# Kernel tuning notes

Hardware: AMD Instinct MI355X
Metric: run time of the kernel (lower is better)

## Reference

```python
import jax, jax.numpy as jnp
import numpy as np

D_MODEL = 1024
NUM_HEADS = 16
D_HEAD = 64  # d_q = d_k = d_v
BATCH = 4
SEQ = 2048


def _trunc_normal(key, shape, std):
    # truncated normal in [-3*std, 3*std], matching nn.init.trunc_normal_
    return jax.random.truncated_normal(key, -3.0, 3.0, shape, dtype=jnp.float32) * std


def setup_inputs() -> dict:
    key = jax.random.key(0)
    k_x, k_q, k_k, k_v, k_o = jax.random.split(key, 5)
    hd = NUM_HEADS * D_HEAD
    s_in = np.sqrt(2.0 / (D_MODEL + hd))
    s_out = np.sqrt(2.0 / (hd + D_MODEL))
    return {
        "in_features": jax.random.normal(k_x, (BATCH, SEQ, D_MODEL), dtype=jnp.float32),
        "w_q": _trunc_normal(k_q, (hd, D_MODEL), s_in),
        "w_k": _trunc_normal(k_k, (hd, D_MODEL), s_in),
        "w_v": _trunc_normal(k_v, (hd, D_MODEL), s_in),
        "w_o": _trunc_normal(k_o, (D_MODEL, hd), s_out),
    }


def reference(in_features, w_q, w_k, w_v, w_o):
    B, S, D = in_features.shape
    H, Dh = NUM_HEADS, D_HEAD
    # QKV projections (weight stored as [out, in])
    q = jnp.einsum('od,bsd->bso', w_q, in_features).reshape(B, S, H, Dh).transpose(0, 2, 1, 3)
    k = jnp.einsum('od,bsd->bso', w_k, in_features).reshape(B, S, H, Dh).transpose(0, 2, 1, 3)
    v = jnp.einsum('od,bsd->bso', w_v, in_features).reshape(B, S, H, Dh).transpose(0, 2, 1, 3)
    # scaled dot-product attention with dense causal mask (as in source)
    att = jnp.einsum('bhqd,bhkd->bhqk', q, k) / jnp.sqrt(jnp.float32(Dh)).astype(q.dtype)
    causal = jnp.tril(jnp.ones((S, S), dtype=bool))
    att = jnp.where(causal, att, -jnp.inf)
    att = jax.nn.softmax(att, axis=-1)
    out = jnp.einsum('bhqk,bhkd->bhqd', att, v)  # [B,H,S,Dh]
    out = out.transpose(0, 2, 1, 3).reshape(B, S, H * Dh)
    return jnp.einsum('od,bsd->bso', w_o, out)
```

## Files before the change

kernel.cpp:

```cpp
#include <hip/hip_runtime.h>
#include <stdint.h>

#define D_MODEL 1024
#define NHEADS  16
#define DHEAD   64
#define BATCH   4
#define SEQ     2048
#define MTOT    (BATCH*SEQ)

typedef unsigned short u16;
typedef uint32_t u32;
typedef __bf16 bf16x8 __attribute__((ext_vector_type(8)));
typedef float  f32x4  __attribute__((ext_vector_type(4)));
typedef float  f32x16 __attribute__((ext_vector_type(16)));
typedef u16    u16x8  __attribute__((ext_vector_type(8)));
typedef u16    u16x4  __attribute__((ext_vector_type(4)));
typedef u32    u32x4  __attribute__((ext_vector_type(4)));

__device__ __forceinline__ u16 f2bf(float f) {
  uint32_t u = __builtin_bit_cast(uint32_t, f);
  u += 0x7fff + ((u >> 16) & 1);
  return (u16)(u >> 16);
}

__device__ __forceinline__ void gll16(const u16* g, u16* lds) {
  __builtin_amdgcn_global_load_lds(
      (__attribute__((address_space(1))) void*)(g),
      (__attribute__((address_space(3))) void*)(lds), 16, 0, 0);
}

__global__ void cvtk(const float4* __restrict__ in, u16x4* __restrict__ out, int n4) {
  const int i = blockIdx.x * blockDim.x + threadIdx.x;
  if (i < n4) {
    const float4 f = in[i];
    u16x4 h;
    h[0] = f2bf(f.x); h[1] = f2bf(f.y); h[2] = f2bf(f.z); h[3] = f2bf(f.w);
    out[i] = h;
  }
}

__global__ void cvtk4(const float4* __restrict__ a, const float4* __restrict__ b,
                      const float4* __restrict__ c, const float4* __restrict__ d,
                      u16x4* __restrict__ out, int n4) {
  const int i = blockIdx.x * blockDim.x + threadIdx.x;
  if (i >= n4) return;
  const float4* src = (blockIdx.y == 0) ? a : (blockIdx.y == 1) ? b
                    : (blockIdx.y == 2) ? c : d;
  const float4 f = src[i];
  u16x4 h;
  h[0] = f2bf(f.x); h[1] = f2bf(f.y); h[2] = f2bf(f.z); h[3] = f2bf(f.w);
  out[(size_t)blockIdx.y * n4 + i] = h;
}

#define QS 8192

#define BARS() __builtin_amdgcn_s_barrier()
#define LGKM0() do { asm volatile("s_waitcnt lgkmcnt(0)" ::: "memory"); \
                     __builtin_amdgcn_sched_barrier(0); } while (0)

#define STG(pbase, roff, t_, slot_) do {                                        \
    gll16((pbase) + (size_t)(roff)*1024 + (t_)*64,      qsm + (slot_)*QS + w*512);        \
    gll16((pbase) + (size_t)((roff)+64)*1024 + (t_)*64, qsm + (slot_)*QS + w*512 + 4096); \
  } while (0)

#define PH_READS_A() do {                                                       \
    _Pragma("unroll")                                                           \
    for (int mf = 0; mf < 8; ++mf) {                                            \
      af0[mf] = *(const bf16x8*)&sA[(mf*16 + r15)*64 + cs0];                    \
      af1[mf] = *(const bf16x8*)&sA[(mf*16 + r15)*64 + cs1];                    \
    }                                                                           \
    _Pragma("unroll")                                                           \
    for (int nf = 0; nf < 4; ++nf)                                              \
      bq[nf] = *(const bf16x8*)&sB[(brow + nf*16 + r15)*64 + cs0];              \
  } while (0)

#define PH_READS_B1() do {                                                      \
    _Pragma("unroll")                                                           \
    for (int nf = 0; nf < 4; ++nf)                                              \
      bq[nf] = *(const bf16x8*)&sB[(brow + nf*16 + r15)*64 + cs1];              \
  } while (0)

#define MM(AF, N0, N1) do {                                                     \
    __builtin_amdgcn_s_setprio(1);                                              \
    _Pragma("unroll")                                                           \
    for (int mf = 0; mf < 8; ++mf) {                                            \
      acc[mf][N0] = __builtin_amdgcn_mfma_f32_16x16x32_bf16(AF[mf], bq[N0],     \
                                                            acc[mf][N0], 0,0,0);\
      acc[mf][N1] = __builtin_amdgcn_mfma_f32_16x16x32_bf16(AF[mf], bq[N1],     \
                                                            acc[mf][N1], 0,0,0);\
    }                                                                           \
    __builtin_amdgcn_s_setprio(0);                                              \
  } while (0)

__global__ __launch_bounds__(512, 2) void gemm_qkv8p(
    const u16* __restrict__ A, const u16* __restrict__ Bw, u16* __restrict__ Out)
{
  extern __shared__ u16 qsm[];
  const int tid = threadIdx.x;
  const int w = tid >> 6, l = tid & 63;
  const int wm = w >> 2, wn = w & 3;
  const int bid = blockIdx.x;
  const int wg = (bid & 7) * 48 + (bid >> 3);
  const int m0 = (wg / 12) * 256, n0 = (wg % 12) * 256;

  const int sr  = 8*w + (l >> 3);
  const int sc8 = ((l & 7) ^ ((l >> 3) & 7)) * 8;
  const u16* pA = A  + (size_t)(m0 + sr) * 1024 + sc8;
  const u16* pB = Bw + (size_t)(n0 + sr) * 1024 + sc8;

  const int r15 = l & 15;
  const int cs0 = (((l >> 4) + 0) ^ (l & 7)) * 8;
  const int cs1 = (((l >> 4) + 4) ^ (l & 7)) * 8;
  const int brow = (wn & 1) * 64;

  f32x4 acc[8][4];
  #pragma unroll
  for (int i = 0; i < 8; ++i)
    #pragma unroll
    for (int j = 0; j < 4; ++j)
      acc[i][j] = f32x4{0.f, 0.f, 0.f, 0.f};

  STG(pA, 0,   0, 0);
  STG(pA, 128, 0, 1);
  STG(pB, 0,   0, 2);
  STG(pB, 128, 0, 3);
  STG(pA, 0,   1, 4);
  STG(pA, 128, 1, 5);
  STG(pB, 0,   1, 6);
  asm volatile("s_waitcnt vmcnt(6)" ::: "memory");
  BARS();
  __builtin_amdgcn_sched_barrier(0);

  #pragma unroll 2
  for (int t = 0; t < 14; ++t) {
    const int p = t & 1, po = p ^ 1;
    const u16* sA = qsm + (size_t)(p*4 + wm) * QS;
    const u16* sB = qsm + (size_t)(p*4 + 2 + (wn >> 1)) * QS;
    bf16x8 af0[8], af1[8], bq[4];
    PH_READS_A();
    STG(pB, 128, t+1, po*4 + 3);
    BARS(); LGKM0();
    MM(af0, 0, 1);
    BARS();
    STG(pA, 0, t+2, p*4 + 0);
    BARS();
    MM(af0, 2, 3);
    BARS();
    PH_READS_B1();
    STG(pA, 128, t+2, p*4 + 1);
    BARS(); LGKM0();
    MM(af1, 0, 1);
    BARS();
    STG(pB, 0, t+2, p*4 + 2);
    BARS();
    MM(af1, 2, 3);
    asm volatile("s_waitcnt vmcnt(6)" ::: "memory");
    BARS();
    __builtin_amdgcn_sched_barrier(0);
  }

  {
    const u16* sA = qsm + (size_t)(0*4 + wm) * QS;
    const u16* sB = qsm + (size_t)(0*4 + 2 + (wn >> 1)) * QS;
    bf16x8 af0[8], af1[8], bq[4];
    PH_READS_A();
    STG(pB, 128, 15, 4 + 3);
    BARS(); LGKM0();
    MM(af0, 0, 1);
    BARS();
    BARS();
    MM(af0, 2, 3);
    BARS();
    PH_READS_B1();
    BARS(); LGKM0();
    MM(af1, 0, 1);
    BARS();
    MM(af1, 2, 3);
    asm volatile("s_waitcnt vmcnt(0)" ::: "memory");
    BARS();
    __builtin_amdgcn_sched_barrier(0);
  }
  {
    const u16* sA = qsm + (size_t)(1*4 + wm) * QS;
    const u16* sB = qsm + (size_t)(1*4 + 2 + (wn >> 1)) * QS;
    bf16x8 af0[8], af1[8], bq[4];
    PH_READS_A();
    MM(af0, 0, 1);
    MM(af0, 2, 3);
    PH_READS_B1();
    MM(af1, 0, 1);
    MM(af1, 2, 3);
  }

  const float scale = (n0 < 1024) ? 0.125f * 1.44269504088896f : 1.0f;
  const int g = l >> 4, c15 = l & 15;
  #pragma unroll
  for (int mf = 0; mf < 8; ++mf) {
    #pragma unroll
    for (int nf = 0; nf < 4; ++nf) {
      #pragma unroll
      for (int j = 0; j < 4; ++j) {
        const int row = m0 + wm*128 + mf*16 + g*4 + j;
        const int col = n0 + wn*64 + nf*16 + c15;
        const int z = col >> 10;
        const int wi = col & 1023;
        const int b = row >> 11, sq = row & (SEQ-1);
        const int h = wi >> 6, dh = wi & (DHEAD-1);
        Out[(size_t)z * MTOT * D_MODEL
            + ((size_t)(b*NHEADS + h) * SEQ + sq) * DHEAD + dh] =
            f2bf(acc[mf][nf][j] * scale);
      }
    }
  }
}

#undef STG
#undef PH_READS_A
#undef PH_READS_B1
#undef MM

#define OSTG(pbase, roff, t_, slot_) do {                                       \
    gll16((pbase) + (size_t)(roff)*1024 + (t_)*64,      osm + (slot_)*QS + w*512);        \
    gll16((pbase) + (size_t)((roff)+64)*1024 + (t_)*64, osm + (slot_)*QS + w*512 + 4096); \
  } while (0)

#define OREADS_P1() do {                                                        \
    _Pragma("unroll")                                                           \
    for (int mf = 0; mf < 8; ++mf) {                                            \
      af0[mf] = *(const bf16x8*)&sA[(mf*16 + r15)*64 + cs0];                    \
      af1[mf] = *(const bf16x8*)&sA[(mf*16 + r15)*64 + cs1];                    \
    }                                                                           \
    _Pragma("unroll")                                                           \
    for (int nf = 0; nf < 2; ++nf)                                              \
      bq[nf] = *(const bf16x8*)&sB[(brow + nf*16 + r15)*64 + cs0];              \
  } while (0)

#define OREADS_P2() do {                                                        \
    _Pragma("unroll")                                                           \
    for (int nf = 0; nf < 2; ++nf)                                              \
      bq[nf] = *(const bf16x8*)&sB[(brow + nf*16 + r15)*64 + cs1];              \
  } while (0)

#define OMM(AF) do {                                                            \
    __builtin_amdgcn_s_setprio(1);                                              \
    _Pragma("unroll")                                                           \
    for (int mf = 0; mf < 8; ++mf) {                                            \
      acc[mf][0] = __builtin_amdgcn_mfma_f32_16x16x32_bf16(AF[mf], bq[0],       \
                                                           acc[mf][0], 0,0,0);  \
      acc[mf][1] = __builtin_amdgcn_mfma_f32_16x16x32_bf16(AF[mf], bq[1],       \
                                                           acc[mf][1], 0,0,0);  \
    }                                                                           \
    __builtin_amdgcn_s_setprio(0);                                              \
  } while (0)

__global__ __launch_bounds__(512, 2) void gemm_o8p(
    const u16* __restrict__ A, const u16* __restrict__ Bw, float* __restrict__ Out)
{
  extern __shared__ u16 osm[];
  const int tid = threadIdx.x;
  const int w = tid >> 6, l = tid & 63;
  const int wm = w >> 2, wn = w & 3;
  const int bid = blockIdx.x;
  const int wg = (bid & 7) * 32 + (bid >> 3);
  const int m0 = (wg >> 3) * 256, n0 = (wg & 7) * 128;

  const int sr  = 8*w + (l >> 3);
  const int sc8 = ((l & 7) ^ ((l >> 3) & 7)) * 8;
  const u16* pA = A  + (size_t)(m0 + sr) * 1024 + sc8;
  const u16* pB = Bw + (size_t)(n0 + sr) * 1024 + sc8;

  const int r15 = l & 15;
  const int cs0 = (((l >> 4) + 0) ^ (l & 7)) * 8;
  const int cs1 = (((l >> 4) + 4) ^ (l & 7)) * 8;
  const int brow = wn * 32;

  f32x4 acc[8][2];
  #pragma unroll
  for (int i = 0; i < 8; ++i) {
    acc[i][0] = f32x4{0.f, 0.f, 0.f, 0.f};
    acc[i][1] = f32x4{0.f, 0.f, 0.f, 0.f};
  }

  OSTG(pA, 0,   0, 0);
  OSTG(pA, 128, 0, 1);
  OSTG(pB, 0,   0, 2);
  OSTG(pA, 0,   1, 3);
  OSTG(pA, 128, 1, 4);
  asm volatile("s_waitcnt vmcnt(4)" ::: "memory");
  BARS();
  __builtin_amdgcn_sched_barrier(0);

  #pragma unroll 2
  for (int t = 0; t < 14; ++t) {
    const int p = t & 1, po = p ^ 1;
    const u16* sA = osm + (size_t)(p*3 + wm) * QS;
    const u16* sB = osm + (size_t)(p*3 + 2) * QS;
    bf16x8 af0[8], af1[8], bq[2];
    OREADS_P1();
    OSTG(pB, 0, t+1, po*3 + 2);
    BARS(); LGKM0();
    OMM(af0);
    BARS();
    OREADS_P2();
    OSTG(pA, 0,   t+2, p*3 + 0);
    OSTG(pA, 128, t+2, p*3 + 1);
    BARS(); LGKM0();
    OMM(af1);
    asm volatile("s_waitcnt vmcnt(4)" ::: "memory");
    BARS();
    __builtin_amdgcn_sched_barrier(0);
  }

  {
    const u16* sA = osm + (size_t)(0*3 + wm) * QS;
    const u16* sB = osm + (size_t)(0*3 + 2) * QS;
    bf16x8 af0[8], af1[8], bq[2];
    OREADS_P1();
    OSTG(pB, 0, 15, 1*3 + 2);
    BARS(); LGKM0();
    OMM(af0);
    BARS();
    OREADS_P2();
    BARS(); LGKM0();
    OMM(af1);
    asm volatile("s_waitcnt vmcnt(0)" ::: "memory");
    BARS();
    __builtin_amdgcn_sched_barrier(0);
  }
  {
    const u16* sA = osm + (size_t)(1*3 + wm) * QS;
    const u16* sB = osm + (size_t)(1*3 + 2) * QS;
    bf16x8 af0[8], af1[8], bq[2];
    OREADS_P1();
    OMM(af0);
    OREADS_P2();
    OMM(af1);
  }

  const int g = l >> 4, c15 = l & 15;
  #pragma unroll
  for (int mf = 0; mf < 8; ++mf) {
    #pragma unroll
    for (int nf = 0; nf < 2; ++nf) {
      #pragma unroll
      for (int j = 0; j < 4; ++j) {
        const int row = m0 + wm*128 + mf*16 + g*4 + j;
        const int col = n0 + wn*32 + nf*16 + c15;
        Out[(size_t)row * D_MODEL + col] = acc[mf][nf][j];
      }
    }
  }
}

#undef OSTG
#undef OREADS_P1
#undef OREADS_P2
#undef OMM

__launch_bounds__(512, 2)
__global__ void attn6_k(const u16* __restrict__ Qb, const u16* __restrict__ Kb_,
                        const u16* __restrict__ Vb_, u16* __restrict__ Oa)
{
  const int tid = threadIdx.x;
  const int w = tid >> 6, l = tid & 63;
  const int q5 = l & 31, hi = l >> 5;
  const int r = blockIdx.x;
  const int bh = (r & 7) * 8 + ((r >> 3) & 7);
  const int pairi = r >> 6;
  const int b = bh >> 4, h = bh & 15;
  const size_t base = (size_t)bh * SEQ * DHEAD;
  const u16* Qg = Qb + base;
  const u16* Kg = Kb_ + base;
  const u16* Vg = Vb_ + base;

  __shared__ __align__(16) u16 smem[32768];

  const int kc = tid & 7, rp = tid >> 3;
  const int vsub = rp >> 5;
  const int rp5 = rp & 31;
  int vIdx32[8];
  #pragma unroll
  for (int e = 0; e < 8; ++e)
    vIdx32[e] = vsub*2048 + (8*kc + e)*32 + ((((rp5 >> 2) ^ kc ^ e) & 7) << 2) + (rp5 & 3);

  const int kr8 = l >> 3;
  const int kkv = 8*w + kr8;
  const int kdc = (l & 7) ^ kr8 ^ w;

  for (int half = 0; half < 2; ++half) {
    const int tq = half ? (7 - pairi) : pairi;
    const int q0w = tq*256 + 32*w;
    const int ntk = (tq + 1) * 2;
    const int ntw = (q0w >> 7) + 1;

    bf16x8 qf[4];
    #pragma unroll
    for (int s = 0; s < 4; ++s)
      qf[s] = *(const bf16x8*)(Qg + (size_t)(q0w + q5)*DHEAD + 16*s + 8*hi);

    f32x16 c0 = {}, c1 = {};
    float mrun = -1e30f, lrun = 0.f;

    {
      #pragma unroll
      for (int h2 = 0; h2 < 2; ++h2)
        gll16(Kg + (size_t)(64*h2 + kkv)*DHEAD + kdc*8, smem + h2*4096 + w*512);
      const u16x8 v0 = *(const u16x8*)(Vg + (size_t)(2*rp)*DHEAD + kc*8);
      const u16x8 v1 = *(const u16x8*)(Vg + (size_t)(2*rp + 1)*DHEAD + kc*8);
      u32* Vd = (u32*)(smem + 16384);
      #pragma unroll
      for (int e = 0; e < 8; ++e)
        Vd[vIdx32[e]] = (u32)v0[e] | ((u32)v1[e] << 16);
    }
    __syncthreads();

    for (int t = 0; t < ntk; ++t) {
      const int cur = t & 1;
      const bool pf = (t + 1 < ntk);
      u16x8 v0, v1;
      if (pf) {
        const int kv1 = (t + 1) * 128;
        v0 = *(const u16x8*)(Vg + (size_t)(kv1 + 2*rp)*DHEAD + kc*8);
        v1 = *(const u16x8*)(Vg + (size_t)(kv1 + 2*rp + 1)*DHEAD + kc*8);
        #pragma unroll
        for (int h2 = 0; h2 < 2; ++h2)
          gll16(Kg + (size_t)(kv1 + 64*h2 + kkv)*DHEAD + kdc*8,
                smem + (cur^1)*8192 + h2*4096 + w*512);
      }

      if (t < ntw) {
        const u16* Kb = smem + cur*8192;
        const u16* Vv = smem + 16384 + cur*8192;

        f32x16 st[4] = {{}, {}, {}, {}};
        __builtin_amdgcn_s_setprio(1);
        #pragma unroll
        for (int kbg = 0; kbg < 4; ++kbg) {
          #pragma unroll
          for (int s = 0; s < 4; ++s) {
            const int slot = ((2*s + hi) ^ (l & 7) ^ ((4*(kbg & 1)) & 7) ^ (q5 >> 3)) & 7;
            const bf16x8 kf = *(const bf16x8*)(Kb + (kbg >> 1)*4096
                                               + ((kbg & 1)*32 + q5)*64 + slot*8);
            st[kbg] = __builtin_amdgcn_mfma_f32_32x32x16_bf16(kf, qf[s], st[kbg], 0, 0, 0);
          }
        }
        __builtin_amdgcn_s_setprio(0);

        if (t == ntw - 1) {
          const int kv0 = t * 128;
          #pragma unroll
          for (int kbg = 0; kbg < 4; ++kbg)
            #pragma unroll
            for (int rr = 0; rr < 16; ++rr) {
              const int kvg = kv0 + 32*kbg + (rr & 3) + 8*(rr >> 2) + 4*hi;
              if (kvg > q0w + q5) st[kbg][rr] = -1e30f;
            }
        }

        float mx = -1e30f;
        #pragma unroll
        for (int kbg = 0; kbg < 4; ++kbg)
          #pragma unroll
          for (int rr = 0; rr < 16; ++rr) mx = fmaxf(mx, st[kbg][rr]);
        mx = fmaxf(mx, __shfl_xor(mx, 32));
        float alpha = 1.0f;
        if (!__all(mx <= mrun + 8.0f)) {
          const float mnew = fmaxf(mrun, mx);
          alpha = __builtin_amdgcn_exp2f(mrun - mnew);
          mrun = mnew;
          #pragma unroll
          for (int rr = 0; rr < 16; ++rr) { c0[rr] *= alpha; c1[rr] *= alpha; }
        }
        float rs = 0.f;
        #pragma unroll
        for (int kbg = 0; kbg < 4; ++kbg)
          #pragma unroll
          for (int rr = 0; rr < 16; ++rr) {
            const float pe = __builtin_amdgcn_exp2f(st[kbg][rr] - mrun);
            st[kbg][rr] = pe;
            rs += pe;
          }
        rs += __shfl_xor(rs, 32);
        lrun = lrun * alpha + rs;

        bf16x8 pb[8];
        #pragma unroll
        for (int kbg = 0; kbg < 4; ++kbg) {
          u32 pw[8];
          #pragma unroll
          for (int i = 0; i < 8; ++i) {
            u32 t0;
            asm("v_cvt_pk_bf16_f32 %0, %1, %2"
                : "=v"(t0) : "v"(st[kbg][2*i]), "v"(st[kbg][2*i+1]));
            pw[i] = t0;
          }
          asm("v_permlane32_swap_b32 %0, %1" : "+v"(pw[0]), "+v"(pw[2]));
          asm("v_permlane32_swap_b32 %0, %1" : "+v"(pw[1]), "+v"(pw[3]));
          asm("v_permlane32_swap_b32 %0, %1" : "+v"(pw[4]), "+v"(pw[6]));
          asm("v_permlane32_swap_b32 %0, %1" : "+v"(pw[5]), "+v"(pw[7]));
          pb[2*kbg]   = __builtin_bit_cast(bf16x8, u32x4{pw[0], pw[1], pw[2], pw[3]});
          pb[2*kbg+1] = __builtin_bit_cast(bf16x8, u32x4{pw[4], pw[5], pw[6], pw[7]});
        }

        __builtin_amdgcn_s_setprio(1);
        #pragma unroll
        for (int h2 = 0; h2 < 2; ++h2) {
          #pragma unroll
          for (int s = 0; s < 4; ++s) {
            {
              const int slot = ((2*s + hi) ^ (l & 7) ^ (q5 >> 3)) & 7;
              const bf16x8 vf = *(const bf16x8*)(Vv + h2*4096 + q5*64 + slot*8);
              c0 = __builtin_amdgcn_mfma_f32_32x32x16_bf16(vf, pb[4*h2 + s], c0, 0, 0, 0);
            }
            {
              const int slot = ((2*s + hi) ^ (l & 7) ^ 4 ^ (q5 >> 3)) & 7;
              const bf16x8 vf = *(const bf16x8*)(Vv + h2*4096 + (32 + q5)*64 + slot*8);
              c1 = __builtin_amdgcn_mfma_f32_32x32x16_bf16(vf, pb[4*h2 + s], c1, 0, 0, 0);
            }
          }
        }
        __builtin_amdgcn_s_setprio(0);
      }

      if (pf) {
        u32* Vd = (u32*)(smem + 16384) + (cur^1)*4096;
        #pragma unroll
        for (int e = 0; e < 8; ++e)
          Vd[vIdx32[e]] = (u32)v0[e] | ((u32)v1[e] << 16);
      }
      __syncthreads();
    }

    const float linv = __builtin_amdgcn_rcpf(lrun);
    #pragma unroll
    for (int Ab = 0; Ab < 2; ++Ab)
      #pragma unroll
      for (int rr = 0; rr < 16; ++rr) {
        const int d = 32*Ab + (rr & 3) + 8*(rr >> 2) + 4*hi;
        smem[w*2048 + q5*64 + (((d >> 3) ^ (q5 & 7)) & 7)*8 + (d & 7)] =
            f2bf((Ab ? c1[rr] : c0[rr]) * linv);
      }
    __syncthreads();
    #pragma unroll
    for (int cc = 0; cc < 4; ++cc) {
      const int dchunk = 4*hi + cc;
      const u16x8 vv = *(const u16x8*)&smem[w*2048 + q5*64 + ((dchunk ^ (q5 & 7)) & 7)*8];
      *(u16x8*)(Oa + (size_t)(b*SEQ + q0w + q5)*D_MODEL + h*DHEAD + 32*hi + 8*cc) = vv;
    }
    __syncthreads();
  }
}

extern "C" void kernel_launch(void* const* d_in, const int* in_sizes, int n_in,
                              void* d_out, int out_size, void* d_ws, size_t ws_size,
                              hipStream_t stream) {
  const float* X  = (const float*)d_in[0];
  const float* Wq = (const float*)d_in[1];
  const float* Wk = (const float*)d_in[2];
  const float* Wv = (const float*)d_in[3];
  const float* Wo = (const float*)d_in[4];

  u16* xb  = (u16*)d_ws;
  u16* wqb = xb  + (size_t)MTOT*D_MODEL;
  u16* wkb = wqb + (size_t)D_MODEL*D_MODEL;
  u16* wvb = wkb + (size_t)D_MODEL*D_MODEL;
  u16* wob = wvb + (size_t)D_MODEL*D_MODEL;
  u16* qkv = wob + (size_t)D_MODEL*D_MODEL;
  u16* att = qkv + (size_t)3*MTOT*D_MODEL;

  (void)hipFuncSetAttribute((const void*)gemm_qkv8p,
                            hipFuncAttributeMaxDynamicSharedMemorySize, 131072);
  (void)hipFuncSetAttribute((const void*)gemm_o8p,
                            hipFuncAttributeMaxDynamicSharedMemorySize, 98304);

  const int nx4 = MTOT*D_MODEL/4;
  const int nw4 = D_MODEL*D_MODEL/4;
  cvtk<<<nx4/256, 256, 0, stream>>>((const float4*)X, (u16x4*)xb, nx4);
  dim3 gc(nw4/256, 4, 1);
  cvtk4<<<gc, 256, 0, stream>>>((const float4*)Wq, (const float4*)Wk,
                                (const float4*)Wv, (const float4*)Wo,
                                (u16x4*)wqb, nw4);

  gemm_qkv8p<<<384, 512, 131072, stream>>>(xb, wqb, qkv);

  attn6_k<<<256, 512, 0, stream>>>(qkv, qkv + (size_t)MTOT*D_MODEL,
                                   qkv + (size_t)2*MTOT*D_MODEL, att);

  gemm_o8p<<<256, 512, 98304, stream>>>(att, wob, (float*)d_out);
}
```

Measured before the change: 153.7 us.

## Retile QKV projection GEMM to 256x192 tiles with 512 workgroups

Changes the fused QKV GEMM tile from 256x256 to 256x192, so the grid grows from 384 to 512 workgroups and fills the 256 CUs in two full waves of 2 blocks per CU, instead of leaving a partial wave. The staging pipeline is restructured: B tiles are loaded as 192 rows per stage with 3 loads per wave, the inner k-step merges into two MFMA phases with fewer barriers, and LDS per block drops to 112KB. The per-column Q scale is now chosen per output column, because a 192-wide tile can straddle the Q/K boundary. Per-tile arithmetic intensity is slightly lower and global traffic for the A operand is higher in exchange for better wave balance.

```diff
diff --git a/kernel.cpp b/kernel.cpp
--- a/kernel.cpp
+++ b/kernel.cpp
@@ -53,46 +53,52 @@
 }
 
 #define QS 8192
-
 #define BARS() __builtin_amdgcn_s_barrier()
 #define LGKM0() do { asm volatile("s_waitcnt lgkmcnt(0)" ::: "memory"); \
                      __builtin_amdgcn_sched_barrier(0); } while (0)
 
-#define STG(pbase, roff, t_, slot_) do {                                        \
-    gll16((pbase) + (size_t)(roff)*1024 + (t_)*64,      qsm + (slot_)*QS + w*512);        \
-    gll16((pbase) + (size_t)((roff)+64)*1024 + (t_)*64, qsm + (slot_)*QS + w*512 + 4096); \
-  } while (0)
-
-#define PH_READS_A() do {                                                       \
-    _Pragma("unroll")                                                           \
-    for (int mf = 0; mf < 8; ++mf) {                                            \
-      af0[mf] = *(const bf16x8*)&sA[(mf*16 + r15)*64 + cs0];                    \
-      af1[mf] = *(const bf16x8*)&sA[(mf*16 + r15)*64 + cs1];                    \
-    }                                                                           \
-    _Pragma("unroll")                                                           \
-    for (int nf = 0; nf < 4; ++nf)                                              \
-      bq[nf] = *(const bf16x8*)&sB[(brow + nf*16 + r15)*64 + cs0];              \
-  } while (0)
-
-#define PH_READS_B1() do {                                                      \
-    _Pragma("unroll")                                                           \
-    for (int nf = 0; nf < 4; ++nf)                                              \
-      bq[nf] = *(const bf16x8*)&sB[(brow + nf*16 + r15)*64 + cs1];              \
-  } while (0)
-
-#define MM(AF, N0, N1) do {                                                     \
-    __builtin_amdgcn_s_setprio(1);                                              \
-    _Pragma("unroll")                                                           \
-    for (int mf = 0; mf < 8; ++mf) {                                            \
-      acc[mf][N0] = __builtin_amdgcn_mfma_f32_16x16x32_bf16(AF[mf], bq[N0],     \
-                                                            acc[mf][N0], 0,0,0);\
-      acc[mf][N1] = __builtin_amdgcn_mfma_f32_16x16x32_bf16(AF[mf], bq[N1],     \
-                                                            acc[mf][N1], 0,0,0);\
-    }                                                                           \
-    __builtin_amdgcn_s_setprio(0);                                              \
-  } while (0)
-
-__global__ __launch_bounds__(512, 2) void gemm_qkv8p(
+#define QP3 28672
+
+#define Q3_ASTG(roff, t_, dstoff) do {                                            \
+    gll16(pA + (size_t)(roff)*1024 + (t_)*64,      qsm + (dstoff) + w*512);       \
+    gll16(pA + (size_t)((roff)+64)*1024 + (t_)*64, qsm + (dstoff) + w*512 + 4096);\
+  } while (0)
+
+#define Q3_BSTG(t_, dstoff) do {                                                  \
+    gll16(pB + (size_t)0*1024  + (t_)*64, qsm + (dstoff) + w*1536);               \
+    gll16(pB + (size_t)8*1024  + (t_)*64, qsm + (dstoff) + w*1536 + 512);         \
+    gll16(pB + (size_t)16*1024 + (t_)*64, qsm + (dstoff) + w*1536 + 1024);        \
+  } while (0)
+
+#define Q3_READS_P1() do {                                                        \
+    _Pragma("unroll")                                                             \
+    for (int mf = 0; mf < 8; ++mf) {                                              \
+      af0[mf] = *(const bf16x8*)&sA[(mf*16 + r15)*64 + cs0];                      \
+      af1[mf] = *(const bf16x8*)&sA[(mf*16 + r15)*64 + cs1];                      \
+    }                                                                             \
+    _Pragma("unroll")                                                             \
+    for (int nf = 0; nf < 3; ++nf)                                                \
+      bq[nf] = *(const bf16x8*)&sB[(brow + nf*16 + r15)*64 + cs0];                \
+  } while (0)
+
+#define Q3_READS_P2() do {                                                        \
+    _Pragma("unroll")                                                             \
+    for (int nf = 0; nf < 3; ++nf)                                                \
+      bq[nf] = *(const bf16x8*)&sB[(brow + nf*16 + r15)*64 + cs1];                \
+  } while (0)
+
+#define Q3_MM(AF) do {                                                            \
+    __builtin_amdgcn_s_setprio(1);                                                \
+    _Pragma("unroll")                                                             \
+    for (int mf = 0; mf < 8; ++mf)                                                \
+      _Pragma("unroll")                                                           \
+      for (int nf = 0; nf < 3; ++nf)                                              \
+        acc[mf][nf] = __builtin_amdgcn_mfma_f32_16x16x32_bf16(AF[mf], bq[nf],     \
+                                                              acc[mf][nf], 0,0,0);\
+    __builtin_amdgcn_s_setprio(0);                                                \
+  } while (0)
+
+__global__ __launch_bounds__(512, 2) void gemm_qkv192(
     const u16* __restrict__ A, const u16* __restrict__ Bw, u16* __restrict__ Out)
 {
   extern __shared__ u16 qsm[];
@@ -100,110 +106,94 @@
   const int w = tid >> 6, l = tid & 63;
   const int wm = w >> 2, wn = w & 3;
   const int bid = blockIdx.x;
-  const int wg = (bid & 7) * 48 + (bid >> 3);
-  const int m0 = (wg / 12) * 256, n0 = (wg % 12) * 256;
-
-  const int sr  = 8*w + (l >> 3);
+  const int wg = (bid & 7) * 64 + (bid >> 3);
+  const int m0 = (wg >> 4) * 256, n0 = (wg & 15) * 192;
+
   const int sc8 = ((l & 7) ^ ((l >> 3) & 7)) * 8;
-  const u16* pA = A  + (size_t)(m0 + sr) * 1024 + sc8;
-  const u16* pB = Bw + (size_t)(n0 + sr) * 1024 + sc8;
+  const u16* pA = A  + (size_t)(m0 + 8*w  + (l >> 3)) * 1024 + sc8;
+  const u16* pB = Bw + (size_t)(n0 + 24*w + (l >> 3)) * 1024 + sc8;
 
   const int r15 = l & 15;
   const int cs0 = (((l >> 4) + 0) ^ (l & 7)) * 8;
   const int cs1 = (((l >> 4) + 4) ^ (l & 7)) * 8;
-  const int brow = (wn & 1) * 64;
-
-  f32x4 acc[8][4];
+  const int brow = wn * 48;
+
+  f32x4 acc[8][3];
   #pragma unroll
   for (int i = 0; i < 8; ++i)
     #pragma unroll
-    for (int j = 0; j < 4; ++j)
+    for (int j = 0; j < 3; ++j)
       acc[i][j] = f32x4{0.f, 0.f, 0.f, 0.f};
 
-  STG(pA, 0,   0, 0);
-  STG(pA, 128, 0, 1);
-  STG(pB, 0,   0, 2);
-  STG(pB, 128, 0, 3);
-  STG(pA, 0,   1, 4);
-  STG(pA, 128, 1, 5);
-  STG(pB, 0,   1, 6);
-  asm volatile("s_waitcnt vmcnt(6)" ::: "memory");
+  Q3_ASTG(0,   0, 0);
+  Q3_ASTG(128, 0, 8192);
+  Q3_BSTG(0, 16384);
+  Q3_ASTG(0,   1, QP3 + 0);
+  Q3_ASTG(128, 1, QP3 + 8192);
+  asm volatile("s_waitcnt vmcnt(4)" ::: "memory");
   BARS();
   __builtin_amdgcn_sched_barrier(0);
 
   #pragma unroll 2
   for (int t = 0; t < 14; ++t) {
     const int p = t & 1, po = p ^ 1;
-    const u16* sA = qsm + (size_t)(p*4 + wm) * QS;
-    const u16* sB = qsm + (size_t)(p*4 + 2 + (wn >> 1)) * QS;
-    bf16x8 af0[8], af1[8], bq[4];
-    PH_READS_A();
-    STG(pB, 128, t+1, po*4 + 3);
-    BARS(); LGKM0();
-    MM(af0, 0, 1);
-    BARS();
-    STG(pA, 0, t+2, p*4 + 0);
-    BARS();
-    MM(af0, 2, 3);
-    BARS();
-    PH_READS_B1();
-    STG(pA, 128, t+2, p*4 + 1);
-    BARS(); LGKM0();
-    MM(af1, 0, 1);
-    BARS();
-    STG(pB, 0, t+2, p*4 + 2);
-    BARS();
-    MM(af1, 2, 3);
-    asm volatile("s_waitcnt vmcnt(6)" ::: "memory");
+    const u16* sA = qsm + (size_t)p*QP3 + (size_t)wm*8192;
+    const u16* sB = qsm + (size_t)p*QP3 + 16384;
+    bf16x8 af0[8], af1[8], bq[3];
+    Q3_READS_P1();
+    Q3_BSTG(t+1, po*QP3 + 16384);
+    BARS(); LGKM0();
+    Q3_MM(af0);
+    BARS();
+    Q3_READS_P2();
+    Q3_ASTG(0,   t+2, p*QP3 + 0);
+    Q3_ASTG(128, t+2, p*QP3 + 8192);
+    BARS(); LGKM0();
+    Q3_MM(af1);
+    asm volatile("s_waitcnt vmcnt(4)" ::: "memory");
     BARS();
     __builtin_amdgcn_sched_barrier(0);
   }
 
   {
-    const u16* sA = qsm + (size_t)(0*4 + wm) * QS;
-    const u16* sB = qsm + (size_t)(0*4 + 2 + (wn >> 1)) * QS;
-    bf16x8 af0[8], af1[8], bq[4];
-    PH_READS_A();
-    STG(pB, 128, 15, 4 + 3);
-    BARS(); LGKM0();
-    MM(af0, 0, 1);
-    BARS();
-    BARS();
-    MM(af0, 2, 3);
-    BARS();
-    PH_READS_B1();
-    BARS(); LGKM0();
-    MM(af1, 0, 1);
-    BARS();
-    MM(af1, 2, 3);
+    const u16* sA = qsm + (size_t)wm*8192;
+    const u16* sB = qsm + 16384;
+    bf16x8 af0[8], af1[8], bq[3];
+    Q3_READS_P1();
+    Q3_BSTG(15, QP3 + 16384);
+    BARS(); LGKM0();
+    Q3_MM(af0);
+    BARS();
+    Q3_READS_P2();
+    BARS(); LGKM0();
+    Q3_MM(af1);
     asm volatile("s_waitcnt vmcnt(0)" ::: "memory");
     BARS();
     __builtin_amdgcn_sched_barrier(0);
   }
   {
-    const u16* sA = qsm + (size_t)(1*4 + wm) * QS;
-    const u16* sB = qsm + (size_t)(1*4 + 2 + (wn >> 1)) * QS;
-    bf16x8 af0[8], af1[8], bq[4];
-    PH_READS_A();
-    MM(af0, 0, 1);
-    MM(af0, 2, 3);
-    PH_READS_B1();
-    MM(af1, 0, 1);
-    MM(af1, 2, 3);
-  }
-
-  const float scale = (n0 < 1024) ? 0.125f * 1.44269504088896f : 1.0f;
+    const u16* sA = qsm + (size_t)QP3 + (size_t)wm*8192;
+    const u16* sB = qsm + (size_t)QP3 + 16384;
+    bf16x8 af0[8], af1[8], bq[3];
+    Q3_READS_P1();
+    Q3_MM(af0);
+    Q3_READS_P2();
+    Q3_MM(af1);
+  }
+
+  const float qs = 0.125f * 1.44269504088896f;
   const int g = l >> 4, c15 = l & 15;
   #pragma unroll
   for (int mf = 0; mf < 8; ++mf) {
     #pragma unroll
-    for (int nf = 0; nf < 4; ++nf) {
+    for (int nf = 0; nf < 3; ++nf) {
       #pragma unroll
       for (int j = 0; j < 4; ++j) {
         const int row = m0 + wm*128 + mf*16 + g*4 + j;
-        const int col = n0 + wn*64 + nf*16 + c15;
+        const int col = n0 + wn*48 + nf*16 + c15;
         const int z = col >> 10;
         const int wi = col & 1023;
+        const float scale = (z == 0) ? qs : 1.0f;
         const int b = row >> 11, sq = row & (SEQ-1);
         const int h = wi >> 6, dh = wi & (DHEAD-1);
         Out[(size_t)z * MTOT * D_MODEL
@@ -214,10 +204,11 @@
   }
 }
 
-#undef STG
-#undef PH_READS_A
-#undef PH_READS_B1
-#undef MM
+#undef Q3_ASTG
+#undef Q3_BSTG
+#undef Q3_READS_P1
+#undef Q3_READS_P2
+#undef Q3_MM
 
 #define OSTG(pbase, roff, t_, slot_) do {                                       \
     gll16((pbase) + (size_t)(roff)*1024 + (t_)*64,      osm + (slot_)*QS + w*512);        \
@@ -568,8 +559,8 @@
   u16* qkv = wob + (size_t)D_MODEL*D_MODEL;
   u16* att = qkv + (size_t)3*MTOT*D_MODEL;
 
-  (void)hipFuncSetAttribute((const void*)gemm_qkv8p,
-                            hipFuncAttributeMaxDynamicSharedMemorySize, 131072);
+  (void)hipFuncSetAttribute((const void*)gemm_qkv192,
+                            hipFuncAttributeMaxDynamicSharedMemorySize, 114688);
   (void)hipFuncSetAttribute((const void*)gemm_o8p,
                             hipFuncAttributeMaxDynamicSharedMemorySize, 98304);
 
@@ -581,7 +572,7 @@
                                 (const float4*)Wv, (const float4*)Wo,
                                 (u16x4*)wqb, nw4);
 
-  gemm_qkv8p<<<384, 512, 131072, stream>>>(xb, wqb, qkv);
+  gemm_qkv192<<<512, 512, 114688, stream>>>(xb, wqb, qkv);
 
   attn6_k<<<256, 512, 0, stream>>>(qkv, qkv + (size_t)MTOT*D_MODEL,
                                    qkv + (size_t)2*MTOT*D_MODEL, att);
```

New measurement: 146.6 us. -4.6%, faster.
